# Performance work log

Hardware: AMD Instinct MI355X
Metric: run time of the kernel (lower is better)

The kernel has to match this reference:

```python
import jax, jax.numpy as jnp
import numpy as np

HEADS = 16
DIMS = [64, 64, 64, 64]  # [d_att(Q), d_att(K), d_ff(V), d_ff(G)]
EPS = 1e-4
P_POW = 2


def _cdist(Q, K):
    # Euclidean pairwise distance via the norm expansion, like torch.cdist.
    # Q: [h, b, t, d], K: [h, b, t, d] -> [h, b, t, t]
    q2 = jnp.sum(Q * Q, axis=-1)  # [h, b, t]
    k2 = jnp.sum(K * K, axis=-1)  # [h, b, t]
    qk = jnp.einsum('hbtd,hbsd->hbts', Q, K)
    d2 = q2[..., :, None] + k2[..., None, :] - 2.0 * qk
    return jnp.sqrt(jnp.maximum(d2, 0.0))


def setup_inputs() -> dict:
    key = jax.random.key(0)
    ks = jax.random.split(key, 4)
    b, t, d_in = 2, 2048, 1024
    d_proj = HEADS * sum(DIMS)  # 4096
    X = jax.random.normal(ks[0], (b, t, d_in), dtype=jnp.float32)
    W_in = jax.random.normal(ks[1], (d_in, d_proj), dtype=jnp.float32) * (d_in ** -0.5)
    b_in = jnp.zeros((d_proj,), dtype=jnp.float32)
    W_out = jax.random.normal(ks[2], (HEADS * DIMS[2], d_in), dtype=jnp.float32) * ((HEADS * DIMS[2]) ** -0.5)
    b_out = jnp.zeros((d_in,), dtype=jnp.float32)
    return {"X": X, "W_in": W_in, "b_in": b_in, "W_out": W_out, "b_out": b_out}


def reference(X, W_in, b_in, W_out, b_out):
    b, t, _ = X.shape
    # multi-head input projection: [b,t,d_in] -> [h,b,t,sum(DIMS)] -> split
    P = X @ W_in + b_in                       # [b, t, h*sum(DIMS)]
    P = P.reshape(b, t, HEADS, sum(DIMS))
    P = jnp.transpose(P, (2, 0, 1, 3))        # [h, b, t, sum(DIMS)]
    splits = np.cumsum(DIMS)[:-1]
    Q, K, V, G = jnp.split(P, splits, axis=-1)
    # Shepard's attention: inverse-power-distance weights
    W = jnp.power(EPS + _cdist(Q, K), -P_POW)         # [h, b, t, t]
    W = W / (EPS + jnp.sum(W, axis=-1, keepdims=True))
    A = jnp.einsum('hbts,hbse->hbte', W, V)           # [h, b, t, e]
    H = G * A                                          # gating
    H = jnp.transpose(H, (1, 2, 0, 3)).reshape(b, t, HEADS * DIMS[2])
    return H @ W_out + b_out
```

## Files before the change

kernel.cpp:

```cpp
#include <hip/hip_runtime.h>
#include <hip/hip_bf16.h>
#include <cstdint>
#include <cstddef>

typedef __bf16 bf16_t;
typedef __attribute__((ext_vector_type(8))) __bf16 bf16x8;
typedef __attribute__((ext_vector_type(4))) float f32x4;
typedef __attribute__((ext_vector_type(16))) float f32x16;
typedef __attribute__((ext_vector_type(4))) unsigned int u32x4;

#define ATT_EPS 1e-4f

__device__ __forceinline__ f32x4 mfma_bf16(bf16x8 a, bf16x8 b, f32x4 c) {
  return __builtin_amdgcn_mfma_f32_16x16x32_bf16(a, b, c, 0, 0, 0);
}
__device__ __forceinline__ f32x16 mfma32(bf16x8 a, bf16x8 b, f32x16 c) {
  return __builtin_amdgcn_mfma_f32_32x32x16_bf16(a, b, c, 0, 0, 0);
}
__device__ __forceinline__ unsigned cvtpk_bf16(float lo, float hi) {
  unsigned r;
  asm("v_cvt_pk_bf16_f32 %0, %1, %2" : "=v"(r) : "v"(lo), "v"(hi));
  return r;
}

#define GLDS16(g, l)                                                          \
  __builtin_amdgcn_global_load_lds(                                           \
      (const __attribute__((address_space(1))) void*)(g),                     \
      (__attribute__((address_space(3))) void*)(l), 16, 0, 0)

__global__ __launch_bounds__(256) void cvt_x_kernel(
    const float* __restrict__ X, bf16_t* __restrict__ Xb, int n8) {
  int i = blockIdx.x * 256 + threadIdx.x;
  if (i >= n8) return;
  f32x4 a = ((const f32x4*)X)[i * 2 + 0];
  f32x4 b = ((const f32x4*)X)[i * 2 + 1];
  bf16x8 o;
  o[0] = (__bf16)a[0]; o[1] = (__bf16)a[1]; o[2] = (__bf16)a[2]; o[3] = (__bf16)a[3];
  o[4] = (__bf16)b[0]; o[5] = (__bf16)b[1]; o[6] = (__bf16)b[2]; o[7] = (__bf16)b[3];
  ((bf16x8*)Xb)[i] = o;
}

__global__ __launch_bounds__(256) void tcvt_kernel(
    const float* __restrict__ W, bf16_t* __restrict__ Wt, int R, int C) {
  __shared__ float T[64][65];
  int tx = threadIdx.x & 63, ty = threadIdx.x >> 6;
  int c0 = blockIdx.x * 64, r0 = blockIdx.y * 64;
#pragma unroll
  for (int i = 0; i < 16; ++i) {
    int rr = ty * 16 + i;
    T[rr][tx] = W[(size_t)(r0 + rr) * C + c0 + tx];
  }
  __syncthreads();
#pragma unroll
  for (int i = 0; i < 16; ++i) {
    int cc = ty * 16 + i;
    Wt[(size_t)(c0 + cc) * R + r0 + tx] = (bf16_t)T[tx][cc];
  }
}

__global__ __launch_bounds__(256) void vt_kernel(
    const bf16_t* __restrict__ P, bf16_t* __restrict__ VtG) {
  __shared__ float T[64][65];
  int h = blockIdx.x;
  int r0 = blockIdx.y * 64;
  int tx = threadIdx.x & 63, ty = threadIdx.x >> 6;
  const bf16_t* src = P + (size_t)r0 * 4096 + h * 256 + 128;
#pragma unroll
  for (int i = 0; i < 16; ++i) {
    int rr = ty * 16 + i;
    T[rr][tx] = (float)src[(size_t)rr * 4096 + tx];
  }
  __syncthreads();
  int ptx = (tx & ~15) | ((tx & 3) | ((tx & 4) << 1) | ((tx & 8) >> 1));
#pragma unroll
  for (int i = 0; i < 16; ++i) {
    int cc = ty * 16 + i;
    VtG[(size_t)(h * 64 + cc) * 4096 + r0 + ptx] = (bf16_t)T[tx][cc];
  }
}

template <int OUTF32>
__global__ __launch_bounds__(256, 2) void gemm_kernel(
    const bf16_t* __restrict__ A, const bf16_t* __restrict__ Bt,
    const float* __restrict__ bias, void* __restrict__ Cout,
    int M, int N, int K) {
  __shared__ bf16_t As[2][128 * 64];
  __shared__ bf16_t Bs[2][128 * 64];
  int tid = threadIdx.x, lane = tid & 63, wv = tid >> 6;
  int l15 = lane & 15, lhi = lane >> 4;
  int NT = N >> 7;
  int nwg = gridDim.x;
  int qq = nwg >> 3;
  int swz = (blockIdx.x & 7) * qq + (blockIdx.x >> 3);
  int tm = swz / NT, tn = swz % NT;
  int m0 = tm << 7, n0 = tn << 7;
  int wm = (wv >> 1) << 6, wn = (wv & 1) << 6;
  int KT = K >> 6;

  auto stage = [&](int buf, int kt) {
    int k0 = kt << 6;
#pragma unroll
    for (int s = 0; s < 4; ++s) {
      int t = s * 256 + tid;
      int row = t >> 3, u = t & 7;
      int cc = (u ^ (row & 7)) << 3;
      GLDS16(A + (size_t)(m0 + row) * K + k0 + cc, &As[buf][t * 8]);
    }
#pragma unroll
    for (int s = 0; s < 4; ++s) {
      int t = s * 256 + tid;
      int row = t >> 3, u = t & 7;
      int cc = (u ^ (row & 7)) << 3;
      GLDS16(Bt + (size_t)(n0 + row) * K + k0 + cc, &Bs[buf][t * 8]);
    }
  };

  f32x4 zero = {0.f, 0.f, 0.f, 0.f};
  f32x4 acc[4][4];
#pragma unroll
  for (int ms = 0; ms < 4; ++ms)
#pragma unroll
    for (int ns = 0; ns < 4; ++ns) acc[ms][ns] = zero;

  stage(0, 0);
  __syncthreads();
  int cur = 0;
  for (int kt = 0; kt < KT; ++kt) {
    if (kt + 1 < KT) stage(cur ^ 1, kt + 1);
#pragma unroll
    for (int ks = 0; ks < 2; ++ks) {
      bf16x8 af[4], bfr[4];
#pragma unroll
      for (int ms = 0; ms < 4; ++ms) {
        int row = wm + ms * 16 + l15;
        af[ms] = *(const bf16x8*)&As[cur][row * 64 + (((ks * 4 + lhi) ^ (row & 7)) << 3)];
      }
#pragma unroll
      for (int ns = 0; ns < 4; ++ns) {
        int col = wn + ns * 16 + l15;
        bfr[ns] = *(const bf16x8*)&Bs[cur][col * 64 + (((ks * 4 + lhi) ^ (col & 7)) << 3)];
      }
#pragma unroll
      for (int ms = 0; ms < 4; ++ms)
#pragma unroll
        for (int ns = 0; ns < 4; ++ns)
          acc[ms][ns] = mfma_bf16(af[ms], bfr[ns], acc[ms][ns]);
    }
    __syncthreads();
    cur ^= 1;
  }

#pragma unroll
  for (int ns = 0; ns < 4; ++ns) {
    int col = n0 + wn + ns * 16 + l15;
    float bv = bias[col];
#pragma unroll
    for (int ms = 0; ms < 4; ++ms) {
      int rowb = m0 + wm + ms * 16 + lhi * 4;
#pragma unroll
      for (int r = 0; r < 4; ++r) {
        float v = acc[ms][ns][r] + bv;
        if (OUTF32)
          ((float*)Cout)[(size_t)(rowb + r) * N + col] = v;
        else
          ((bf16_t*)Cout)[(size_t)(rowb + r) * N + col] = (bf16_t)v;
      }
    }
  }
}

__global__ __launch_bounds__(256) void norms_kernel(
    const bf16_t* __restrict__ P, float* __restrict__ Q2, float* __restrict__ K2) {
  int tid = threadIdx.x, lane = tid & 63, wv = tid >> 6;
  int wg = blockIdx.x * 4 + wv;
  int h = wg >> 9, rb = wg & 511;
  int r = rb * 8 + (lane >> 3), ch = lane & 7;
  const bf16_t* base = P + (size_t)r * 4096 + h * 256 + ch * 8;
  bf16x8 qv = *(const bf16x8*)base;
  bf16x8 kv = *(const bf16x8*)(base + 64);
  float sq = 0.f, sk = 0.f;
#pragma unroll
  for (int j = 0; j < 8; ++j) {
    float a = (float)qv[j];
    sq += a * a;
    float c = (float)kv[j];
    sk += c * c;
  }
#pragma unroll
  for (int m = 1; m <= 4; m <<= 1) {
    sq += __shfl_xor(sq, m);
    sk += __shfl_xor(sk, m);
  }
  if (ch == 0) {
    Q2[h * 4096 + r] = sq;
    K2[h * 4096 + r] = sk;
  }
}

__global__ __launch_bounds__(512, 4) void attn_kernel(
    const bf16_t* __restrict__ P, const bf16_t* __restrict__ VtG,
    const float* __restrict__ Q2, const float* __restrict__ K2,
    bf16_t* __restrict__ H) {
  __shared__ bf16_t Ks[128 * 64];
  __shared__ bf16_t Vts[64 * 128];
  __shared__ float Comb[4][64][33];
  __shared__ float invLds[4][32];

  int tid = threadIdx.x, lane = tid & 63, wv = tid >> 6;
  int l31 = lane & 31, hi = lane >> 5, hi4 = hi * 4;
  int qw = wv & 3, sw = wv >> 2;
  int sOff = sw * 64;
  int swz = (blockIdx.x & 7) * 64 + (blockIdx.x >> 3);
  int hb = swz >> 4, qt = swz & 15;
  int h = hb >> 1, b = hb & 1;
  int rowbase = b * 2048;
  const bf16_t* Pq = P + (size_t)rowbase * 4096 + h * 256;
  const bf16_t* Pk = Pq + 64;
  const bf16_t* Pg = Pq + 192;
  const bf16_t* Vg = VtG + (size_t)h * 64 * 4096 + rowbase;
  const float* Q2g = Q2 + h * 4096 + rowbase;
  const float* K2g = K2 + h * 4096 + rowbase;
  int q0 = qt * 128 + qw * 32;

  bf16x8 qm[4];
#pragma unroll
  for (int db = 0; db < 4; ++db) {
    bf16x8 q = *(const bf16x8*)(Pq + (size_t)(q0 + l31) * 4096 + db * 16 + hi * 8);
    u32x4 u = *(u32x4*)&q;
    u = (u ^ 0x80008000u) + 0x00800080u;
    qm[db] = *(bf16x8*)&u;
  }
  float q2s = Q2g[q0 + l31];

  f32x16 nacc0, nacc1;
#pragma unroll
  for (int r = 0; r < 16; ++r) { nacc0[r] = 0.f; nacc1[r] = 0.f; }
  float dacc0 = 0.f, dacc1 = 0.f;

  for (int st = 0; st < 16; ++st) {
    int s0 = st * 128;
    __syncthreads();
#pragma unroll
    for (int s4 = 0; s4 < 2; ++s4) {
      int t = s4 * 512 + tid;
      int row = t >> 3, u = t & 7;
      int cc = (u ^ (row & 7)) << 3;
      GLDS16(Pk + (size_t)(s0 + row) * 4096 + cc, &Ks[t * 8]);
    }
#pragma unroll
    for (int s4 = 0; s4 < 2; ++s4) {
      int t = s4 * 512 + tid;
      int row = t >> 4, u = t & 15;
      int cc = (u ^ (row & 7)) << 3;
      GLDS16(Vg + (size_t)row * 4096 + s0 + cc, &Vts[t * 8]);
    }
    const float* K2t = K2g + s0 + sOff;
    f32x4 k2a[4];
#pragma unroll
    for (int g = 0; g < 4; ++g) k2a[g] = *(const f32x4*)(K2t + g * 8 + hi4);
    __syncthreads();

#pragma unroll
    for (int sb = 0; sb < 2; ++sb) {
      int sbase = sOff + sb * 32;
      f32x16 D;
#pragma unroll
      for (int g = 0; g < 4; ++g)
#pragma unroll
        for (int j = 0; j < 4; ++j) D[g * 4 + j] = k2a[g][j] + q2s;
      if (sb == 0) {
#pragma unroll
        for (int g = 0; g < 4; ++g) k2a[g] = *(const f32x4*)(K2t + 32 + g * 8 + hi4);
      }
#pragma unroll
      for (int db = 0; db < 4; ++db) {
        int srow = sbase + l31;
        bf16x8 kf = *(const bf16x8*)&Ks[srow * 64 + (((db * 2 + hi) ^ (srow & 7)) << 3)];
        D = mfma32(kf, qm[db], D);
      }
      float p[16];
#pragma unroll
      for (int r = 0; r < 16; ++r) {
        float w = __builtin_amdgcn_rcpf(fmaxf(D[r], 1e-12f));
        if (r & 1) dacc1 += w; else dacc0 += w;
        p[r] = w;
      }
      u32x4 w0v = {cvtpk_bf16(p[0], p[1]), cvtpk_bf16(p[2], p[3]),
                   cvtpk_bf16(p[4], p[5]), cvtpk_bf16(p[6], p[7])};
      u32x4 w1v = {cvtpk_bf16(p[8], p[9]), cvtpk_bf16(p[10], p[11]),
                   cvtpk_bf16(p[12], p[13]), cvtpk_bf16(p[14], p[15])};
      bf16x8 pa0 = *(bf16x8*)&w0v;
      bf16x8 pa1 = *(bf16x8*)&w1v;
      int e = l31;
      int ciB = (sOff >> 3) + sb * 4;
      bf16x8 vb00 = *(const bf16x8*)&Vts[e * 128 + (((ciB + 0 + hi) ^ (e & 7)) << 3)];
      bf16x8 vb01 = *(const bf16x8*)&Vts[(e + 32) * 128 + (((ciB + 0 + hi) ^ ((e + 32) & 7)) << 3)];
      bf16x8 vb10 = *(const bf16x8*)&Vts[e * 128 + (((ciB + 2 + hi) ^ (e & 7)) << 3)];
      bf16x8 vb11 = *(const bf16x8*)&Vts[(e + 32) * 128 + (((ciB + 2 + hi) ^ ((e + 32) & 7)) << 3)];
      nacc0 = mfma32(pa0, vb00, nacc0);
      nacc1 = mfma32(pa0, vb01, nacc1);
      nacc0 = mfma32(pa1, vb10, nacc0);
      nacc1 = mfma32(pa1, vb11, nacc1);
    }
  }

  __syncthreads();
  if (sw == 1) {
#pragma unroll
    for (int r = 0; r < 16; ++r) {
      Comb[qw][lane][r] = nacc0[r];
      Comb[qw][lane][16 + r] = nacc1[r];
    }
    Comb[qw][lane][32] = dacc0 + dacc1;
  }
  __syncthreads();
  if (sw == 0) {
    float dacc = dacc0 + dacc1 + Comb[qw][lane][32];
#pragma unroll
    for (int r = 0; r < 16; ++r) {
      nacc0[r] += Comb[qw][lane][r];
      nacc1[r] += Comb[qw][lane][16 + r];
    }
    dacc += __shfl_xor(dacc, 32);
    float inv = __builtin_amdgcn_rcpf(ATT_EPS + dacc);
    if (lane < 32) invLds[qw][l31] = inv;
    __builtin_amdgcn_s_waitcnt(0);
#pragma unroll
    for (int r = 0; r < 16; ++r) {
      int q = (r & 3) + 8 * (r >> 2) + hi4;
      int tq = q0 + q;
      float iv = invLds[qw][q];
      float g0 = (float)Pg[(size_t)tq * 4096 + l31];
      float g1 = (float)Pg[(size_t)tq * 4096 + 32 + l31];
      H[(size_t)(rowbase + tq) * 1024 + h * 64 + l31] = (bf16_t)(g0 * nacc0[r] * iv);
      H[(size_t)(rowbase + tq) * 1024 + h * 64 + 32 + l31] = (bf16_t)(g1 * nacc1[r] * iv);
    }
  }
}

extern "C" void kernel_launch(void* const* d_in, const int* in_sizes, int n_in,
                              void* d_out, int out_size, void* d_ws, size_t ws_size,
                              hipStream_t stream) {
  const float* X     = (const float*)d_in[0];
  const float* W_in  = (const float*)d_in[1];
  const float* b_in  = (const float*)d_in[2];
  const float* W_out = (const float*)d_in[3];
  const float* b_out = (const float*)d_in[4];

  char* ws = (char*)d_ws;
  bf16_t* Xb  = (bf16_t*)(ws);
  bf16_t* VtG = (bf16_t*)(ws);
  bf16_t* WbT = (bf16_t*)(ws + ((size_t)8  << 20));
  bf16_t* WoT = (bf16_t*)(ws + ((size_t)16 << 20));
  bf16_t* Pb  = (bf16_t*)(ws + ((size_t)18 << 20));
  bf16_t* Hb  = (bf16_t*)(ws + ((size_t)50 << 20));
  float*  Q2  = (float*) (ws + ((size_t)58 << 20));
  float*  K2  = (float*) (ws + ((size_t)59 << 20));

  cvt_x_kernel<<<2048, 256, 0, stream>>>(X, Xb, 4096 * 1024 / 8);
  tcvt_kernel<<<dim3(64, 16), 256, 0, stream>>>(W_in, WbT, 1024, 4096);
  tcvt_kernel<<<dim3(16, 16), 256, 0, stream>>>(W_out, WoT, 1024, 1024);
  gemm_kernel<0><<<1024, 256, 0, stream>>>(Xb, WbT, b_in, Pb, 4096, 4096, 1024);
  norms_kernel<<<2048, 256, 0, stream>>>(Pb, Q2, K2);
  vt_kernel<<<dim3(16, 64), 256, 0, stream>>>(Pb, VtG);
  attn_kernel<<<512, 512, 0, stream>>>(Pb, VtG, Q2, K2, Hb);
  gemm_kernel<1><<<256, 256, 0, stream>>>(Hb, WoT, b_out, d_out, 4096, 1024, 1024);
}
```

Baseline: 145.7 us.

## Double-buffer K/V tiles in LDS and raise wave priority around MFMAs

The attention loop now keeps two LDS buffers for the K and V^T tiles. It issues the global-to-LDS loads for the next key tile before computing on the current one, so each iteration needs one barrier instead of two. The combine scratch shares storage with the tile buffers through a union, which keeps total LDS about the same. The MFMA sequences are also wrapped in s_setprio raises. The prefetch should overlap memory latency with compute, at the cost of more in-flight loads and reliance on the end-of-iteration barrier to drain them.

```diff
diff --git a/kernel.cpp b/kernel.cpp
--- a/kernel.cpp
+++ b/kernel.cpp
@@ -201,9 +201,10 @@
     const bf16_t* __restrict__ P, const bf16_t* __restrict__ VtG,
     const float* __restrict__ Q2, const float* __restrict__ K2,
     bf16_t* __restrict__ H) {
-  __shared__ bf16_t Ks[128 * 64];
-  __shared__ bf16_t Vts[64 * 128];
-  __shared__ float Comb[4][64][33];
+  __shared__ union Smem {
+    struct { bf16_t Ks[2][128 * 64]; bf16_t Vts[2][64 * 128]; } l;
+    float Comb[4][64][33];
+  } sm;
   __shared__ float invLds[4][32];
 
   int tid = threadIdx.x, lane = tid & 63, wv = tid >> 6;
@@ -222,6 +223,23 @@
   const float* K2g = K2 + h * 4096 + rowbase;
   int q0 = qt * 128 + qw * 32;
 
+  auto stageKV = [&](int buf, int s0) {
+#pragma unroll
+    for (int s4 = 0; s4 < 2; ++s4) {
+      int t = s4 * 512 + tid;
+      int row = t >> 3, u = t & 7;
+      int cc = (u ^ (row & 7)) << 3;
+      GLDS16(Pk + (size_t)(s0 + row) * 4096 + cc, &sm.l.Ks[buf][t * 8]);
+    }
+#pragma unroll
+    for (int s4 = 0; s4 < 2; ++s4) {
+      int t = s4 * 512 + tid;
+      int row = t >> 4, u = t & 15;
+      int cc = (u ^ (row & 7)) << 3;
+      GLDS16(Vg + (size_t)row * 4096 + s0 + cc, &sm.l.Vts[buf][t * 8]);
+    }
+  };
+
   bf16x8 qm[4];
 #pragma unroll
   for (int db = 0; db < 4; ++db) {
@@ -237,29 +255,22 @@
   for (int r = 0; r < 16; ++r) { nacc0[r] = 0.f; nacc1[r] = 0.f; }
   float dacc0 = 0.f, dacc1 = 0.f;
 
+  stageKV(0, 0);
+  __syncthreads();
+
   for (int st = 0; st < 16; ++st) {
+    int cur = st & 1;
     int s0 = st * 128;
-    __syncthreads();
-#pragma unroll
-    for (int s4 = 0; s4 < 2; ++s4) {
-      int t = s4 * 512 + tid;
-      int row = t >> 3, u = t & 7;
-      int cc = (u ^ (row & 7)) << 3;
-      GLDS16(Pk + (size_t)(s0 + row) * 4096 + cc, &Ks[t * 8]);
-    }
-#pragma unroll
-    for (int s4 = 0; s4 < 2; ++s4) {
-      int t = s4 * 512 + tid;
-      int row = t >> 4, u = t & 15;
-      int cc = (u ^ (row & 7)) << 3;
-      GLDS16(Vg + (size_t)row * 4096 + s0 + cc, &Vts[t * 8]);
-    }
     const float* K2t = K2g + s0 + sOff;
-    f32x4 k2a[4];
+    f32x4 k2a[4], k2b[4];
 #pragma unroll
     for (int g = 0; g < 4; ++g) k2a[g] = *(const f32x4*)(K2t + g * 8 + hi4);
-    __syncthreads();
-
+#pragma unroll
+    for (int g = 0; g < 4; ++g) k2b[g] = *(const f32x4*)(K2t + 32 + g * 8 + hi4);
+    if (st + 1 < 16) stageKV(cur ^ 1, s0 + 128);
+
+    const bf16_t* KsC = sm.l.Ks[cur];
+    const bf16_t* VtC = sm.l.Vts[cur];
 #pragma unroll
     for (int sb = 0; sb < 2; ++sb) {
       int sbase = sOff + sb * 32;
@@ -267,17 +278,16 @@
 #pragma unroll
       for (int g = 0; g < 4; ++g)
 #pragma unroll
-        for (int j = 0; j < 4; ++j) D[g * 4 + j] = k2a[g][j] + q2s;
-      if (sb == 0) {
-#pragma unroll
-        for (int g = 0; g < 4; ++g) k2a[g] = *(const f32x4*)(K2t + 32 + g * 8 + hi4);
-      }
+        for (int j = 0; j < 4; ++j)
+          D[g * 4 + j] = (sb ? k2b[g][j] : k2a[g][j]) + q2s;
+      __builtin_amdgcn_s_setprio(1);
 #pragma unroll
       for (int db = 0; db < 4; ++db) {
         int srow = sbase + l31;
-        bf16x8 kf = *(const bf16x8*)&Ks[srow * 64 + (((db * 2 + hi) ^ (srow & 7)) << 3)];
+        bf16x8 kf = *(const bf16x8*)&KsC[srow * 64 + (((db * 2 + hi) ^ (srow & 7)) << 3)];
         D = mfma32(kf, qm[db], D);
       }
+      __builtin_amdgcn_s_setprio(0);
       float p[16];
 #pragma unroll
       for (int r = 0; r < 16; ++r) {
@@ -293,33 +303,35 @@
       bf16x8 pa1 = *(bf16x8*)&w1v;
       int e = l31;
       int ciB = (sOff >> 3) + sb * 4;
-      bf16x8 vb00 = *(const bf16x8*)&Vts[e * 128 + (((ciB + 0 + hi) ^ (e & 7)) << 3)];
-      bf16x8 vb01 = *(const bf16x8*)&Vts[(e + 32) * 128 + (((ciB + 0 + hi) ^ ((e + 32) & 7)) << 3)];
-      bf16x8 vb10 = *(const bf16x8*)&Vts[e * 128 + (((ciB + 2 + hi) ^ (e & 7)) << 3)];
-      bf16x8 vb11 = *(const bf16x8*)&Vts[(e + 32) * 128 + (((ciB + 2 + hi) ^ ((e + 32) & 7)) << 3)];
+      bf16x8 vb00 = *(const bf16x8*)&VtC[e * 128 + (((ciB + 0 + hi) ^ (e & 7)) << 3)];
+      bf16x8 vb01 = *(const bf16x8*)&VtC[(e + 32) * 128 + (((ciB + 0 + hi) ^ ((e + 32) & 7)) << 3)];
+      bf16x8 vb10 = *(const bf16x8*)&VtC[e * 128 + (((ciB + 2 + hi) ^ (e & 7)) << 3)];
+      bf16x8 vb11 = *(const bf16x8*)&VtC[(e + 32) * 128 + (((ciB + 2 + hi) ^ ((e + 32) & 7)) << 3)];
+      __builtin_amdgcn_s_setprio(1);
       nacc0 = mfma32(pa0, vb00, nacc0);
       nacc1 = mfma32(pa0, vb01, nacc1);
       nacc0 = mfma32(pa1, vb10, nacc0);
       nacc1 = mfma32(pa1, vb11, nacc1);
-    }
-  }
-
-  __syncthreads();
+      __builtin_amdgcn_s_setprio(0);
+    }
+    __syncthreads();
+  }
+
   if (sw == 1) {
 #pragma unroll
     for (int r = 0; r < 16; ++r) {
-      Comb[qw][lane][r] = nacc0[r];
-      Comb[qw][lane][16 + r] = nacc1[r];
-    }
-    Comb[qw][lane][32] = dacc0 + dacc1;
+      sm.Comb[qw][lane][r] = nacc0[r];
+      sm.Comb[qw][lane][16 + r] = nacc1[r];
+    }
+    sm.Comb[qw][lane][32] = dacc0 + dacc1;
   }
   __syncthreads();
   if (sw == 0) {
-    float dacc = dacc0 + dacc1 + Comb[qw][lane][32];
+    float dacc = dacc0 + dacc1 + sm.Comb[qw][lane][32];
 #pragma unroll
     for (int r = 0; r < 16; ++r) {
-      nacc0[r] += Comb[qw][lane][r];
-      nacc1[r] += Comb[qw][lane][16 + r];
+      nacc0[r] += sm.Comb[qw][lane][r];
+      nacc1[r] += sm.Comb[qw][lane][16 + r];
     }
     dacc += __shfl_xor(dacc, 32);
     float inv = __builtin_amdgcn_rcpf(ATT_EPS + dacc);
```

Result: slower. 162.9 us (+11.8%).
